# Optimization experiments

Hardware: AMD Instinct MI355X
Metric: run time of the kernel (lower is better)

Reference implementation:

```python
import jax, jax.numpy as jnp
import numpy as np

NUM_HEADS = 8
DIM = 256
SCALE = (DIM // NUM_HEADS) ** -0.5  # head_dim = dim // nhead = 32


def setup_inputs() -> dict:
    key = jax.random.key(0)
    k1, k2, k3, k4, k5 = jax.random.split(key, 5)
    B, N = 1, 4096
    qk = jax.random.normal(k1, (B, N, 3 * DIM), dtype=jnp.float32)
    v_cls = jax.random.normal(k2, (B, N, 2 * DIM), dtype=jnp.float32)
    masks = jax.random.uniform(k3, (B, N, N), dtype=jnp.float32)
    # torch Linear weights stored as [in, out] for x @ W
    W_qk = jax.random.normal(k4, (3 * DIM, 6 * DIM), dtype=jnp.float32) * (3 * DIM) ** -0.5
    W_v = jax.random.normal(k5, (2 * DIM, 2 * DIM), dtype=jnp.float32) * (2 * DIM) ** -0.5
    return {"qk": qk, "v_cls": v_cls, "masks": masks, "W_qk": W_qk, "W_v": W_v}


def reference(qk, v_cls, masks, W_qk, W_v):
    B, N, C_qk = qk.shape
    C_cls = v_cls.shape[-1]
    H = NUM_HEADS
    hd_qk = C_qk // H   # 96
    hd_v = C_cls // H   # 64

    # qk projection: [B,N,6*dim] -> (2,B,H,N,hd_qk)
    proj = (qk @ W_qk).reshape(B, N, 2, H, hd_qk).transpose(2, 0, 3, 1, 4)
    q, k = proj[0], proj[1]                      # [B,H,N,hd_qk]
    v = (v_cls @ W_v).reshape(B, N, H, hd_v).transpose(0, 2, 1, 3)  # [B,H,N,hd_v]

    attn = jnp.einsum('bhnd,bhmd->bhnm', q, k) * SCALE
    attn = jax.nn.softmax(attn, axis=-1)

    # post-softmax mask-mul and renorm by mask-sum and head count
    m = masks[:, None]                           # [B,1,N,N] broadcast over heads
    attn = attn * m / (H * jnp.sum(m, axis=-1, keepdims=True))
    # attn_drop with p=0.0 is identity in eval

    x_cls = jnp.einsum('bhnm,bhmd->bhnd', attn, v)
    return x_cls.transpose(0, 2, 1, 3).reshape(B, N, C_cls)
```

## Files before the change

### kernel.cpp

```cpp
#include <hip/hip_runtime.h>

typedef __attribute__((ext_vector_type(8))) _Float16 half8;
typedef __attribute__((ext_vector_type(4))) _Float16 half4;
typedef __attribute__((ext_vector_type(2))) _Float16 half2;
typedef __attribute__((ext_vector_type(2))) __fp16 fp16x2;
typedef __attribute__((ext_vector_type(4))) float f32x4;

#define N_SEQ 4096
#define HD_QK 96
#define HD_V  64
#define NHEADS 8
#define QSCALE 0.25505545556f
#define ESHIFT 8.0f

union PKC { fp16x2 p; half2 h; };

__device__ inline half2 pk_cvt(float a, float b) {
    PKC u;
    u.p = __builtin_amdgcn_cvt_pkrtz(a, b);
    return u.h;
}

__device__ inline half8 cvt8(float4 a, float4 b) {
    half8 h;
    h[0] = (_Float16)a.x; h[1] = (_Float16)a.y; h[2] = (_Float16)a.z; h[3] = (_Float16)a.w;
    h[4] = (_Float16)b.x; h[5] = (_Float16)b.y; h[6] = (_Float16)b.z; h[7] = (_Float16)b.w;
    return h;
}

__device__ inline void cast_blk(const float* __restrict__ in, _Float16* __restrict__ out,
                                int blk, int t) {
    size_t i = ((size_t)blk * 256 + t) * 8;
    float4 a = *(const float4*)(in + i);
    float4 b = *(const float4*)(in + i + 4);
    *(half8*)(out + i) = cvt8(a, b);
}

__global__ __launch_bounds__(256) void prep(
    const float* __restrict__ qk, const float* __restrict__ v_cls,
    const float* __restrict__ masks, const float* __restrict__ W_qk,
    const float* __restrict__ W_v,
    _Float16* __restrict__ Xh, _Float16* __restrict__ Vch,
    _Float16* __restrict__ Msw, float* __restrict__ Msum,
    _Float16* __restrict__ Wqkt, _Float16* __restrict__ Wvt)
{
    __shared__ float tile[32][33];
    const int bx = blockIdx.x, t = threadIdx.x;
    if (bx < 1536) {
        cast_blk(qk, Xh, bx, t);
    } else if (bx < 2560) {
        cast_blk(v_cls, Vch, bx - 1536, t);
    } else if (bx < 3968) {
        const bool big = bx < 3712;
        const int id = big ? bx - 2560 : bx - 3712;
        const int nx = big ? 48 : 16;
        const int C = big ? 1536 : 512, R = big ? 768 : 512;
        const float* in = big ? W_qk : W_v;
        _Float16* out = big ? Wqkt : Wvt;
        int cx = id % nx, cy = id / nx;
        int tx = t & 31, ty = t >> 5;
        int c0 = cx * 32, r0 = cy * 32;
        for (int k = 0; k < 4; k++)
            tile[ty + 8 * k][tx] = in[(size_t)(r0 + ty + 8 * k) * C + c0 + tx];
        __syncthreads();
        for (int k = 0; k < 4; k++)
            out[(size_t)(c0 + ty + 8 * k) * R + r0 + tx] = (_Float16)tile[tx][ty + 8 * k];
    } else {
        const int m = bx - 3968;
        const int q = m >> 1;
        const int k0 = (m & 1) * 2048 + t * 8;
        const float* src = masks + (size_t)q * N_SEQ + k0;
        float4 a = *(const float4*)src;
        float4 b = *(const float4*)(src + 4);
        const int q0b = q >> 6, l15 = q & 15, nt = (q >> 4) & 3;
        const int kb = k0 >> 6, wsl = (k0 >> 4) & 3, qd = (k0 >> 2) & 3;
        _Float16* dst = Msw + ((size_t)(q0b * 64 + kb) * 4 + wsl) * 1024
                            + l15 * 64 + qd * 16 + nt * 4;
        half4 h0 = {(_Float16)a.x, (_Float16)a.y, (_Float16)a.z, (_Float16)a.w};
        half4 h1 = {(_Float16)b.x, (_Float16)b.y, (_Float16)b.z, (_Float16)b.w};
        *(half4*)dst = h0;
        *(half4*)(dst + 16) = h1;
        float s = (a.x + a.y) + (a.z + a.w) + (b.x + b.y) + (b.z + b.w);
        for (int off = 1; off < 64; off <<= 1) s += __shfl_xor(s, off);
        if ((t & 63) == 0) atomicAdd(&Msum[q], s);
    }
}

__global__ __launch_bounds__(256) void proj_fused(
    const _Float16* __restrict__ Xh, const _Float16* __restrict__ Vch,
    const _Float16* __restrict__ Wqkt, const _Float16* __restrict__ Wvt,
    _Float16* __restrict__ Qh, _Float16* __restrict__ Kh,
    _Float16* __restrict__ Vtg)
{
    __shared__ _Float16 smem[2 * 128 * 72];
    _Float16 (*Xs)[72] = (_Float16 (*)[72])smem;
    _Float16 (*Ws)[72] = (_Float16 (*)[72])(smem + 128 * 72);

    const int t = threadIdx.x;
    const int lane = t & 63, wv = t >> 6;
    const int quad = lane >> 4, l15 = lane & 15;
    const bool qkmode = blockIdx.x < 12;
    const int n0 = qkmode ? blockIdx.x * 128 : (blockIdx.x - 12) * 128;
    const int row0 = blockIdx.y * 128;
    const int K = qkmode ? 768 : 512;
    const _Float16* X = qkmode ? Xh : Vch;
    const _Float16* Wt = qkmode ? Wqkt : Wvt;

    const int mB = (wv & 1) * 64, nB = (wv >> 1) * 64;
    const int sr = t >> 1, sk = (t & 1) * 32;

    const f32x4 fzero = {0.f, 0.f, 0.f, 0.f};
    f32x4 acc[4][4];
    for (int i = 0; i < 4; i++)
        for (int j = 0; j < 4; j++) acc[i][j] = fzero;

    for (int k0 = 0; k0 < K; k0 += 64) {
        __syncthreads();
        {
            const _Float16* xp = X + (size_t)(row0 + sr) * K + k0 + sk;
            *(half8*)&Xs[sr][sk]      = *(const half8*)xp;
            *(half8*)&Xs[sr][sk + 8]  = *(const half8*)(xp + 8);
            *(half8*)&Xs[sr][sk + 16] = *(const half8*)(xp + 16);
            *(half8*)&Xs[sr][sk + 24] = *(const half8*)(xp + 24);
            const _Float16* wp = Wt + (size_t)(n0 + sr) * K + k0 + sk;
            *(half8*)&Ws[sr][sk]      = *(const half8*)wp;
            *(half8*)&Ws[sr][sk + 8]  = *(const half8*)(wp + 8);
            *(half8*)&Ws[sr][sk + 16] = *(const half8*)(wp + 16);
            *(half8*)&Ws[sr][sk + 24] = *(const half8*)(wp + 24);
        }
        __syncthreads();
        for (int c = 0; c < 2; c++) {
            half8 af[4], bf[4];
            for (int i = 0; i < 4; i++)
                af[i] = *(const half8*)&Xs[mB + 16 * i + l15][c * 32 + quad * 8];
            for (int j = 0; j < 4; j++)
                bf[j] = *(const half8*)&Ws[nB + 16 * j + l15][c * 32 + quad * 8];
            for (int i = 0; i < 4; i++)
                for (int j = 0; j < 4; j++)
                    acc[i][j] = __builtin_amdgcn_mfma_f32_16x16x32_f16(af[i], bf[j], acc[i][j], 0, 0, 0);
        }
    }

    __syncthreads();
    _Float16 (*Ct)[136] = (_Float16 (*)[136])smem;
    for (int j = 0; j < 4; j++) {
        int col = n0 + nB + 16 * j + l15;
        float scl = (qkmode && col < 768) ? QSCALE : 1.0f;
        for (int i = 0; i < 4; i++)
            for (int r = 0; r < 4; r++)
                Ct[mB + 16 * i + quad * 4 + r][nB + 16 * j + l15] =
                    (_Float16)(acc[i][j][r] * scl);
    }
    __syncthreads();

    if (qkmode) {
        for (int e = 0; e < 8; e++) {
            int id = e * 256 + t;
            int row = id >> 4, cc = id & 15;
            int col = n0 + cc * 8;
            int w = col >= 768 ? 1 : 0;
            int rem = col - w * 768;
            int h = rem / 96, d = rem - h * 96;
            _Float16* dst = w ? Kh : Qh;
            *(half8*)&dst[((size_t)h * N_SEQ + row0 + row) * HD_QK + d] =
                *(const half8*)&Ct[row][cc * 8];
        }
    } else {
        for (int e = 0; e < 4; e++) {
            int id = e * 256 + t;
            int col = id >> 3, rc = id & 7;
            int c = n0 + col;
            int h = c >> 6, d = c & 63;
            half8 v0, v1;
            for (int k = 0; k < 8; k++) {
                v0[k] = Ct[rc * 16 + k][col];
                v1[k] = Ct[rc * 16 + 8 + k][col];
            }
            _Float16* dst = &Vtg[((size_t)h * HD_V + d) * N_SEQ + row0 + rc * 16];
            *(half8*)dst = v0;
            *(half8*)(dst + 8) = v1;
        }
    }
}

__global__ __launch_bounds__(256, 3) void flash_attn(
    const _Float16* __restrict__ Qh, const _Float16* __restrict__ Kh,
    const _Float16* __restrict__ Vtg, const _Float16* __restrict__ Msw,
    _Float16* __restrict__ Owsh, float* __restrict__ Lws)
{
    __shared__ __align__(16) float Ob[2][64][68];
    __shared__ float Lb[2][64];

    const int t = threadIdx.x;
    const int lane = t & 63, w = t >> 6;
    const int quad = lane >> 4, l15 = lane & 15;
    const int bx = blockIdx.x;
    const int q0b = bx & 63;
    const int hz = bx >> 6;
    const int head = hz & 7;
    const int z = hz >> 3;
    const int q0 = q0b * 64;
    const int kb0 = 21 * z, kbE = (z == 2) ? 64 : kb0 + 21;

    half8 qf[3][4];
    for (int nt = 0; nt < 4; nt++) {
        const _Float16* qp = Qh + ((size_t)head * N_SEQ + q0 + 16 * nt + l15) * HD_QK + 8 * quad;
        for (int c = 0; c < 3; c++)
            qf[c][nt] = *(const half8*)(qp + 32 * c);
    }

    const _Float16* kbase = Kh + ((size_t)head * N_SEQ + 16 * w + l15) * HD_QK + 8 * quad;
    const _Float16* vbase = Vtg + ((size_t)head * HD_V + l15) * N_SEQ + 16 * w + 4 * quad;
    const _Float16* mbase = Msw + ((size_t)(q0b * 64 + kb0) * 4 + w) * 1024
                                + (l15 * 4 + quad) * 16;

    const f32x4 fzero = {0.f, 0.f, 0.f, 0.f};
    f32x4 oacc[4][4];
    for (int nt = 0; nt < 4; nt++)
        for (int v = 0; v < 4; v++) oacc[nt][v] = fzero;
    float lsum[4] = {0.f, 0.f, 0.f, 0.f};

    half8 kf[3];
    half4 vf[4];
    half8 m01, m23;
    {
        const _Float16* kp = kbase + (size_t)kb0 * 64 * HD_QK;
        for (int c = 0; c < 3; c++) kf[c] = *(const half8*)(kp + 32 * c);
        const _Float16* vp = vbase + kb0 * 64;
        for (int v = 0; v < 4; v++) vf[v] = *(const half4*)(vp + (size_t)(16 * v) * N_SEQ);
        m01 = *(const half8*)mbase;
        m23 = *(const half8*)(mbase + 8);
    }

    for (int kb = kb0; kb < kbE; kb++) {
        const int kn = (kb + 1 < kbE) ? kb + 1 : kb;

        f32x4 sT[4];
        for (int nt = 0; nt < 4; nt++) sT[nt] = fzero;
        for (int c = 0; c < 3; c++)
            for (int nt = 0; nt < 4; nt++)
                sT[nt] = __builtin_amdgcn_mfma_f32_16x16x32_f16(kf[c], qf[c][nt], sT[nt], 0, 0, 0);
        {
            const _Float16* kp = kbase + (size_t)kn * 64 * HD_QK;
            for (int c = 0; c < 3; c++) kf[c] = *(const half8*)(kp + 32 * c);
        }

        half4 af[4];
        {
            half2 mh[8];
            for (int i = 0; i < 4; i++) {
                mh[i]     = half2{m01[2 * i], m01[2 * i + 1]};
                mh[4 + i] = half2{m23[2 * i], m23[2 * i + 1]};
            }
            for (int nt = 0; nt < 4; nt++) {
                float p0 = exp2f(sT[nt][0] - ESHIFT);
                float p1 = exp2f(sT[nt][1] - ESHIFT);
                float p2 = exp2f(sT[nt][2] - ESHIFT);
                float p3 = exp2f(sT[nt][3] - ESHIFT);
                lsum[nt] += (p0 + p1) + (p2 + p3);
                half2 lo = pk_cvt(p0, p1) * mh[2 * nt];
                half2 hi = pk_cvt(p2, p3) * mh[2 * nt + 1];
                af[nt] = half4{lo[0], lo[1], hi[0], hi[1]};
            }
        }
        {
            const _Float16* mp = mbase + (size_t)(kn - kb0) * 4096;
            m01 = *(const half8*)mp;
            m23 = *(const half8*)(mp + 8);
        }

        for (int nt = 0; nt < 4; nt++)
            for (int v = 0; v < 4; v++)
                oacc[nt][v] = __builtin_amdgcn_mfma_f32_16x16x16f16(af[nt], vf[v], oacc[nt][v], 0, 0, 0);
        {
            const _Float16* vp = vbase + kn * 64;
            for (int v = 0; v < 4; v++) vf[v] = *(const half4*)(vp + (size_t)(16 * v) * N_SEQ);
        }
    }

    for (int nt = 0; nt < 4; nt++) {
        lsum[nt] += __shfl_xor(lsum[nt], 16);
        lsum[nt] += __shfl_xor(lsum[nt], 32);
    }

    if (w & 1) {
        for (int nt = 0; nt < 4; nt++) {
            for (int v = 0; v < 4; v++)
                for (int r = 0; r < 4; r++)
                    Ob[w >> 1][16 * nt + 4 * quad + r][16 * v + l15] = oacc[nt][v][r];
            if (quad == 0) Lb[w >> 1][16 * nt + l15] = lsum[nt];
        }
    }
    __syncthreads();
    if (!(w & 1)) {
        for (int nt = 0; nt < 4; nt++) {
            for (int v = 0; v < 4; v++)
                for (int r = 0; r < 4; r++)
                    Ob[w >> 1][16 * nt + 4 * quad + r][16 * v + l15] += oacc[nt][v][r];
            if (quad == 0) Lb[w >> 1][16 * nt + l15] += lsum[nt];
        }
    }
    __syncthreads();

    {
        int row = t >> 2, c0 = (t & 3) * 16;
        _Float16* obase = Owsh + (size_t)z * N_SEQ * 512 + (size_t)(q0 + row) * 512
                          + head * HD_V + c0;
        for (int g = 0; g < 2; g++) {
            half8 h;
            for (int j = 0; j < 8; j++)
                h[j] = (_Float16)(Ob[0][row][c0 + 8 * g + j] + Ob[1][row][c0 + 8 * g + j]);
            *(half8*)(obase + 8 * g) = h;
        }
        if (t < 64)
            Lws[((size_t)z * NHEADS + head) * N_SEQ + q0 + t] = Lb[0][t] + Lb[1][t];
    }
}

__global__ __launch_bounds__(256) void finalize(
    const _Float16* __restrict__ Owsh, const float* __restrict__ Lws,
    const float* __restrict__ Msum, float* __restrict__ out)
{
    const size_t ZSTR = (size_t)N_SEQ * 512;
    size_t o = ((size_t)blockIdx.x * 256 + threadIdx.x) * 8;
    int q = (int)(o >> 9);
    int head = (int)((o & 511) >> 6);
    half8 p0 = *(const half8*)(Owsh + o);
    half8 p1 = *(const half8*)(Owsh + ZSTR + o);
    half8 p2 = *(const half8*)(Owsh + 2 * ZSTR + o);
    float l = Lws[(size_t)head * N_SEQ + q]
            + Lws[((size_t)NHEADS + head) * N_SEQ + q]
            + Lws[((size_t)2 * NHEADS + head) * N_SEQ + q];
    float inv = 1.0f / (l * (float)NHEADS * Msum[q]);
    float4 r0, r1;
    r0.x = ((float)p0[0] + (float)p1[0] + (float)p2[0]) * inv;
    r0.y = ((float)p0[1] + (float)p1[1] + (float)p2[1]) * inv;
    r0.z = ((float)p0[2] + (float)p1[2] + (float)p2[2]) * inv;
    r0.w = ((float)p0[3] + (float)p1[3] + (float)p2[3]) * inv;
    r1.x = ((float)p0[4] + (float)p1[4] + (float)p2[4]) * inv;
    r1.y = ((float)p0[5] + (float)p1[5] + (float)p2[5]) * inv;
    r1.z = ((float)p0[6] + (float)p1[6] + (float)p2[6]) * inv;
    r1.w = ((float)p0[7] + (float)p1[7] + (float)p2[7]) * inv;
    *(float4*)(out + o) = r0;
    *(float4*)(out + o + 4) = r1;
}

extern "C" void kernel_launch(void* const* d_in, const int* in_sizes, int n_in,
                              void* d_out, int out_size, void* d_ws, size_t ws_size,
                              hipStream_t stream) {
    const float* qk    = (const float*)d_in[0];
    const float* v_cls = (const float*)d_in[1];
    const float* masks = (const float*)d_in[2];
    const float* W_qk  = (const float*)d_in[3];
    const float* W_v   = (const float*)d_in[4];
    float* out = (float*)d_out;

    char* wsp = (char*)d_ws;
    _Float16* Xh   = (_Float16*)(wsp);
    _Float16* Vch  = (_Float16*)(wsp + (size_t)6291456);
    _Float16* Wqkt = (_Float16*)(wsp + (size_t)10485760);
    _Float16* Wvt  = (_Float16*)(wsp + (size_t)12845056);
    _Float16* Owsh = (_Float16*)(wsp);
    size_t off = 13631488;
    auto allocB = [&](size_t bytes) { char* p = wsp + off; off += (bytes + 255) & ~(size_t)255; return p; };
    _Float16* Qh   = (_Float16*)allocB((size_t)NHEADS * N_SEQ * HD_QK * 2);
    _Float16* Kh   = (_Float16*)allocB((size_t)NHEADS * N_SEQ * HD_QK * 2);
    _Float16* Vtg  = (_Float16*)allocB((size_t)NHEADS * HD_V * N_SEQ * 2);
    _Float16* Msw  = (_Float16*)allocB((size_t)N_SEQ * N_SEQ * 2);
    float*    Msum = (float*)allocB((size_t)N_SEQ * 4);
    float*    Lws  = (float*)allocB((size_t)3 * NHEADS * N_SEQ * 4);
    (void)ws_size;

    dim3 blk(256);
    (void)hipMemsetAsync(Msum, 0, N_SEQ * sizeof(float), stream);
    prep<<<dim3(12160), blk, 0, stream>>>(
        qk, v_cls, masks, W_qk, W_v, Xh, Vch, Msw, Msum, Wqkt, Wvt);

    proj_fused<<<dim3(16, N_SEQ / 128), blk, 0, stream>>>(
        Xh, Vch, Wqkt, Wvt, Qh, Kh, Vtg);

    flash_attn<<<dim3(1536), blk, 0, stream>>>(
        Qh, Kh, Vtg, Msw, Owsh, Lws);

    finalize<<<dim3((N_SEQ * 512) / (256 * 8)), blk, 0, stream>>>(
        Owsh, Lws, Msum, out);
}
```

Before: 281.5 us.

## Software-pipeline QK MFMA of next block with softmax and PV of previous block

Restructures the attention inner loop so the QK^T MFMAs for key block j run while exp/mask/PV work for block j-1 proceeds, using two ping-pong score register sets unrolled by two. This lets matrix-core work overlap the exp and convert ALU work. It also folds the exp shift into the MFMA accumulator init, dropping one subtract per element. The cost is an extra set of score registers, which adds pressure at the 3-waves launch bound.

```diff
diff --git a/kernel.cpp b/kernel.cpp
--- a/kernel.cpp
+++ b/kernel.cpp
@@ -183,6 +183,69 @@
     }
 }
 
+
+#define QK_MFMA(CUR)                                                          \
+    for (int c = 0; c < 3; c++)                                               \
+        for (int nt = 0; nt < 4; nt++)                                        \
+            CUR[nt] = __builtin_amdgcn_mfma_f32_16x16x32_f16(                 \
+                kf[c], qf[c][nt], (c == 0) ? minit : CUR[nt], 0, 0, 0);
+
+#define EXP_BLK(ST)                                                           \
+    {                                                                         \
+        half2 mh[8];                                                          \
+        for (int i = 0; i < 4; i++) {                                         \
+            mh[i]     = half2{m01[2 * i], m01[2 * i + 1]};                    \
+            mh[4 + i] = half2{m23[2 * i], m23[2 * i + 1]};                    \
+        }                                                                     \
+        for (int nt = 0; nt < 4; nt++) {                                      \
+            float p0 = exp2f(ST[nt][0]);                                      \
+            float p1 = exp2f(ST[nt][1]);                                      \
+            float p2 = exp2f(ST[nt][2]);                                      \
+            float p3 = exp2f(ST[nt][3]);                                      \
+            lsum[nt] += (p0 + p1) + (p2 + p3);                                \
+            half2 lo = pk_cvt(p0, p1) * mh[2 * nt];                           \
+            half2 hi = pk_cvt(p2, p3) * mh[2 * nt + 1];                       \
+            af[nt] = half4{lo[0], lo[1], hi[0], hi[1]};                       \
+        }                                                                     \
+    }
+
+#define PV_BLK                                                                \
+    for (int nt = 0; nt < 4; nt++)                                            \
+        for (int v = 0; v < 4; v++)                                           \
+            oacc[nt][v] = __builtin_amdgcn_mfma_f32_16x16x16f16(              \
+                af[nt], vf[v], oacc[nt][v], 0, 0, 0);
+
+#define STEP(CUR, PREV, J)                                                    \
+    do {                                                                      \
+        QK_MFMA(CUR);                                                         \
+        {                                                                     \
+            int kn_ = ((J) + 1 < kbE) ? (J) + 1 : (J);                        \
+            const _Float16* kp_ = kbase + (size_t)kn_ * 64 * HD_QK;           \
+            for (int c = 0; c < 3; c++)                                       \
+                kf[c] = *(const half8*)(kp_ + 32 * c);                        \
+        }                                                                     \
+        half4 af[4];                                                          \
+        EXP_BLK(PREV);                                                        \
+        {                                                                     \
+            const _Float16* mp_ = mbase + (size_t)((J) - kb0) * 4096;         \
+            m01 = *(const half8*)mp_;                                         \
+            m23 = *(const half8*)(mp_ + 8);                                   \
+        }                                                                     \
+        PV_BLK;                                                               \
+        {                                                                     \
+            const _Float16* vp_ = vbase + (J) * 64;                           \
+            for (int v = 0; v < 4; v++)                                       \
+                vf[v] = *(const half4*)(vp_ + (size_t)(16 * v) * N_SEQ);      \
+        }                                                                     \
+    } while (0)
+
+#define FINAL_BLK(ST)                                                         \
+    do {                                                                      \
+        half4 af[4];                                                          \
+        EXP_BLK(ST);                                                          \
+        PV_BLK;                                                               \
+    } while (0)
+
 __global__ __launch_bounds__(256, 3) void flash_attn(
     const _Float16* __restrict__ Qh, const _Float16* __restrict__ Kh,
     const _Float16* __restrict__ Vtg, const _Float16* __restrict__ Msw,
@@ -215,6 +278,7 @@
                                 + (l15 * 4 + quad) * 16;
 
     const f32x4 fzero = {0.f, 0.f, 0.f, 0.f};
+    const f32x4 minit = {-ESHIFT, -ESHIFT, -ESHIFT, -ESHIFT};
     f32x4 oacc[4][4];
     for (int nt = 0; nt < 4; nt++)
         for (int v = 0; v < 4; v++) oacc[nt][v] = fzero;
@@ -232,50 +296,24 @@
         m23 = *(const half8*)(mbase + 8);
     }
 
-    for (int kb = kb0; kb < kbE; kb++) {
-        const int kn = (kb + 1 < kbE) ? kb + 1 : kb;
-
-        f32x4 sT[4];
-        for (int nt = 0; nt < 4; nt++) sT[nt] = fzero;
-        for (int c = 0; c < 3; c++)
-            for (int nt = 0; nt < 4; nt++)
-                sT[nt] = __builtin_amdgcn_mfma_f32_16x16x32_f16(kf[c], qf[c][nt], sT[nt], 0, 0, 0);
-        {
-            const _Float16* kp = kbase + (size_t)kn * 64 * HD_QK;
-            for (int c = 0; c < 3; c++) kf[c] = *(const half8*)(kp + 32 * c);
-        }
-
-        half4 af[4];
-        {
-            half2 mh[8];
-            for (int i = 0; i < 4; i++) {
-                mh[i]     = half2{m01[2 * i], m01[2 * i + 1]};
-                mh[4 + i] = half2{m23[2 * i], m23[2 * i + 1]};
-            }
-            for (int nt = 0; nt < 4; nt++) {
-                float p0 = exp2f(sT[nt][0] - ESHIFT);
-                float p1 = exp2f(sT[nt][1] - ESHIFT);
-                float p2 = exp2f(sT[nt][2] - ESHIFT);
-                float p3 = exp2f(sT[nt][3] - ESHIFT);
-                lsum[nt] += (p0 + p1) + (p2 + p3);
-                half2 lo = pk_cvt(p0, p1) * mh[2 * nt];
-                half2 hi = pk_cvt(p2, p3) * mh[2 * nt + 1];
-                af[nt] = half4{lo[0], lo[1], hi[0], hi[1]};
-            }
-        }
-        {
-            const _Float16* mp = mbase + (size_t)(kn - kb0) * 4096;
-            m01 = *(const half8*)mp;
-            m23 = *(const half8*)(mp + 8);
-        }
-
-        for (int nt = 0; nt < 4; nt++)
-            for (int v = 0; v < 4; v++)
-                oacc[nt][v] = __builtin_amdgcn_mfma_f32_16x16x16f16(af[nt], vf[v], oacc[nt][v], 0, 0, 0);
-        {
-            const _Float16* vp = vbase + kn * 64;
-            for (int v = 0; v < 4; v++) vf[v] = *(const half4*)(vp + (size_t)(16 * v) * N_SEQ);
-        }
+    f32x4 sTA[4], sTB[4];
+    QK_MFMA(sTA);
+    {
+        const _Float16* kp = kbase + (size_t)(kb0 + 1) * 64 * HD_QK;
+        for (int c = 0; c < 3; c++) kf[c] = *(const half8*)(kp + 32 * c);
+    }
+
+    const int nsteps = kbE - kb0 - 1;
+    int j = kb0 + 1;
+    for (int s = 0; s + 1 < nsteps; s += 2) {
+        STEP(sTB, sTA, j); ++j;
+        STEP(sTA, sTB, j); ++j;
+    }
+    if (nsteps & 1) {
+        STEP(sTB, sTA, j);
+        FINAL_BLK(sTB);
+    } else {
+        FINAL_BLK(sTA);
     }
 
     for (int nt = 0; nt < 4; nt++) {
@@ -308,14 +346,20 @@
                           + head * HD_V + c0;
         for (int g = 0; g < 2; g++) {
             half8 h;
-            for (int j = 0; j < 8; j++)
-                h[j] = (_Float16)(Ob[0][row][c0 + 8 * g + j] + Ob[1][row][c0 + 8 * g + j]);
+            for (int j2 = 0; j2 < 8; j2++)
+                h[j2] = (_Float16)(Ob[0][row][c0 + 8 * g + j2] + Ob[1][row][c0 + 8 * g + j2]);
             *(half8*)(obase + 8 * g) = h;
         }
         if (t < 64)
             Lws[((size_t)z * NHEADS + head) * N_SEQ + q0 + t] = Lb[0][t] + Lb[1][t];
     }
 }
+
+#undef QK_MFMA
+#undef EXP_BLK
+#undef PV_BLK
+#undef STEP
+#undef FINAL_BLK
 
 __global__ __launch_bounds__(256) void finalize(
     const _Float16* __restrict__ Owsh, const float* __restrict__ Lws,
```

Result: slower. 454.2 us (+61.4%).

## Software-pipeline QK MFMA with softmax exp across key blocks, fold shift into init

Applied to the files above, without the earlier changes.

Restructures the attention loop so the QK^T MFMAs for the next key block are issued while the exp/mask work of the current block runs, using a prologue and epilogue. The exp shift is folded into the MFMA accumulator initial value, which removes a subtraction per element. Explicit unroll pragmas are added throughout. This is meant to hide MFMA latency behind VALU transcendental work, at the cost of extra live registers for a second score tile.

```diff
diff --git a/kernel.cpp b/kernel.cpp
--- a/kernel.cpp
+++ b/kernel.cpp
@@ -203,8 +203,10 @@
     const int kb0 = 21 * z, kbE = (z == 2) ? 64 : kb0 + 21;
 
     half8 qf[3][4];
+#pragma unroll
     for (int nt = 0; nt < 4; nt++) {
         const _Float16* qp = Qh + ((size_t)head * N_SEQ + q0 + 16 * nt + l15) * HD_QK + 8 * quad;
+#pragma unroll
         for (int c = 0; c < 3; c++)
             qf[c][nt] = *(const half8*)(qp + 32 * c);
     }
@@ -215,8 +217,11 @@
                                 + (l15 * 4 + quad) * 16;
 
     const f32x4 fzero = {0.f, 0.f, 0.f, 0.f};
+    const f32x4 minit = {-ESHIFT, -ESHIFT, -ESHIFT, -ESHIFT};
     f32x4 oacc[4][4];
+#pragma unroll
     for (int nt = 0; nt < 4; nt++)
+#pragma unroll
         for (int v = 0; v < 4; v++) oacc[nt][v] = fzero;
     float lsum[4] = {0.f, 0.f, 0.f, 0.f};
 
@@ -225,57 +230,100 @@
     half8 m01, m23;
     {
         const _Float16* kp = kbase + (size_t)kb0 * 64 * HD_QK;
+#pragma unroll
         for (int c = 0; c < 3; c++) kf[c] = *(const half8*)(kp + 32 * c);
         const _Float16* vp = vbase + kb0 * 64;
+#pragma unroll
         for (int v = 0; v < 4; v++) vf[v] = *(const half4*)(vp + (size_t)(16 * v) * N_SEQ);
         m01 = *(const half8*)mbase;
         m23 = *(const half8*)(mbase + 8);
     }
 
-    for (int kb = kb0; kb < kbE; kb++) {
-        const int kn = (kb + 1 < kbE) ? kb + 1 : kb;
-
-        f32x4 sT[4];
-        for (int nt = 0; nt < 4; nt++) sT[nt] = fzero;
-        for (int c = 0; c < 3; c++)
-            for (int nt = 0; nt < 4; nt++)
-                sT[nt] = __builtin_amdgcn_mfma_f32_16x16x32_f16(kf[c], qf[c][nt], sT[nt], 0, 0, 0);
+    f32x4 sT[4];
+#pragma unroll
+    for (int nt = 0; nt < 4; nt++) {
+        f32x4 s = __builtin_amdgcn_mfma_f32_16x16x32_f16(kf[0], qf[0][nt], minit, 0, 0, 0);
+        s = __builtin_amdgcn_mfma_f32_16x16x32_f16(kf[1], qf[1][nt], s, 0, 0, 0);
+        s = __builtin_amdgcn_mfma_f32_16x16x32_f16(kf[2], qf[2][nt], s, 0, 0, 0);
+        sT[nt] = s;
+    }
+    {
+        const _Float16* kp = kbase + (size_t)(kb0 + 1) * 64 * HD_QK;
+#pragma unroll
+        for (int c = 0; c < 3; c++) kf[c] = *(const half8*)(kp + 32 * c);
+    }
+
+    for (int j = kb0 + 1; j < kbE; j++) {
+        half4 af[4];
+        half2 mh[8];
+#pragma unroll
+        for (int i = 0; i < 4; i++) {
+            mh[i]     = half2{m01[2 * i], m01[2 * i + 1]};
+            mh[4 + i] = half2{m23[2 * i], m23[2 * i + 1]};
+        }
+#pragma unroll
+        for (int nt = 0; nt < 4; nt++) {
+            f32x4 s = __builtin_amdgcn_mfma_f32_16x16x32_f16(kf[0], qf[0][nt], minit, 0, 0, 0);
+            s = __builtin_amdgcn_mfma_f32_16x16x32_f16(kf[1], qf[1][nt], s, 0, 0, 0);
+            s = __builtin_amdgcn_mfma_f32_16x16x32_f16(kf[2], qf[2][nt], s, 0, 0, 0);
+            float p0 = exp2f(sT[nt][0]);
+            float p1 = exp2f(sT[nt][1]);
+            float p2 = exp2f(sT[nt][2]);
+            float p3 = exp2f(sT[nt][3]);
+            lsum[nt] += (p0 + p1) + (p2 + p3);
+            half2 lo = pk_cvt(p0, p1) * mh[2 * nt];
+            half2 hi = pk_cvt(p2, p3) * mh[2 * nt + 1];
+            af[nt] = half4{lo[0], lo[1], hi[0], hi[1]};
+            sT[nt] = s;
+        }
         {
+            int kn = (j + 1 < kbE) ? j + 1 : j;
             const _Float16* kp = kbase + (size_t)kn * 64 * HD_QK;
+#pragma unroll
             for (int c = 0; c < 3; c++) kf[c] = *(const half8*)(kp + 32 * c);
         }
-
-        half4 af[4];
         {
-            half2 mh[8];
-            for (int i = 0; i < 4; i++) {
-                mh[i]     = half2{m01[2 * i], m01[2 * i + 1]};
-                mh[4 + i] = half2{m23[2 * i], m23[2 * i + 1]};
-            }
-            for (int nt = 0; nt < 4; nt++) {
-                float p0 = exp2f(sT[nt][0] - ESHIFT);
-                float p1 = exp2f(sT[nt][1] - ESHIFT);
-                float p2 = exp2f(sT[nt][2] - ESHIFT);
-                float p3 = exp2f(sT[nt][3] - ESHIFT);
-                lsum[nt] += (p0 + p1) + (p2 + p3);
-                half2 lo = pk_cvt(p0, p1) * mh[2 * nt];
-                half2 hi = pk_cvt(p2, p3) * mh[2 * nt + 1];
-                af[nt] = half4{lo[0], lo[1], hi[0], hi[1]};
-            }
-        }
-        {
-            const _Float16* mp = mbase + (size_t)(kn - kb0) * 4096;
+            const _Float16* mp = mbase + (size_t)(j - kb0) * 4096;
             m01 = *(const half8*)mp;
             m23 = *(const half8*)(mp + 8);
         }
-
+#pragma unroll
         for (int nt = 0; nt < 4; nt++)
+#pragma unroll
             for (int v = 0; v < 4; v++)
                 oacc[nt][v] = __builtin_amdgcn_mfma_f32_16x16x16f16(af[nt], vf[v], oacc[nt][v], 0, 0, 0);
         {
-            const _Float16* vp = vbase + kn * 64;
-            for (int v = 0; v < 4; v++) vf[v] = *(const half4*)(vp + (size_t)(16 * v) * N_SEQ);
-        }
+            const _Float16* vp = vbase + (size_t)j * 64;
+#pragma unroll
+            for (int v = 0; v < 4; v++)
+                vf[v] = *(const half4*)(vp + (size_t)(16 * v) * N_SEQ);
+        }
+    }
+
+    {
+        half4 af[4];
+        half2 mh[8];
+#pragma unroll
+        for (int i = 0; i < 4; i++) {
+            mh[i]     = half2{m01[2 * i], m01[2 * i + 1]};
+            mh[4 + i] = half2{m23[2 * i], m23[2 * i + 1]};
+        }
+#pragma unroll
+        for (int nt = 0; nt < 4; nt++) {
+            float p0 = exp2f(sT[nt][0]);
+            float p1 = exp2f(sT[nt][1]);
+            float p2 = exp2f(sT[nt][2]);
+            float p3 = exp2f(sT[nt][3]);
+            lsum[nt] += (p0 + p1) + (p2 + p3);
+            half2 lo = pk_cvt(p0, p1) * mh[2 * nt];
+            half2 hi = pk_cvt(p2, p3) * mh[2 * nt + 1];
+            af[nt] = half4{lo[0], lo[1], hi[0], hi[1]};
+        }
+#pragma unroll
+        for (int nt = 0; nt < 4; nt++)
+#pragma unroll
+            for (int v = 0; v < 4; v++)
+                oacc[nt][v] = __builtin_amdgcn_mfma_f32_16x16x16f16(af[nt], vf[v], oacc[nt][v], 0, 0, 0);
     }
 
     for (int nt = 0; nt < 4; nt++) {
@@ -308,8 +356,8 @@
                           + head * HD_V + c0;
         for (int g = 0; g < 2; g++) {
             half8 h;
-            for (int j = 0; j < 8; j++)
-                h[j] = (_Float16)(Ob[0][row][c0 + 8 * g + j] + Ob[1][row][c0 + 8 * g + j]);
+            for (int j2 = 0; j2 < 8; j2++)
+                h[j2] = (_Float16)(Ob[0][row][c0 + 8 * g + j2] + Ob[1][row][c0 + 8 * g + j2]);
             *(half8*)(obase + 8 * g) = h;
         }
         if (t < 64)
```

After: 310.8 us. 10.4% more time.

## Double-buffer K/V/mask register prefetch two blocks ahead and fold shift into MFMA init

Applied to the files above, without the earlier changes.

Restructures the attention inner loop to keep two register sets of K, V and mask fragments, loading block j+2 while computing block j, with the loop unrolled by two and a remainder step. The -ESHIFT subtraction is folded into the QK accumulator's initial value, and the three QK MFMAs per tile are chained per nt. The aim is to hide global-load latency behind more compute. The extra registers may reduce occupancy at the launch bound of 3 blocks per CU or cause spills.

```diff
diff --git a/kernel.cpp b/kernel.cpp
--- a/kernel.cpp
+++ b/kernel.cpp
@@ -183,6 +183,60 @@
     }
 }
 
+
+#define FA_ITER(KF, VF, M01, M23, J)                                          \
+    do {                                                                      \
+        f32x4 sT[4];                                                          \
+        for (int nt = 0; nt < 4; nt++) {                                      \
+            f32x4 s = __builtin_amdgcn_mfma_f32_16x16x32_f16(KF[0], qf[0][nt], minit, 0, 0, 0); \
+            s = __builtin_amdgcn_mfma_f32_16x16x32_f16(KF[1], qf[1][nt], s, 0, 0, 0); \
+            s = __builtin_amdgcn_mfma_f32_16x16x32_f16(KF[2], qf[2][nt], s, 0, 0, 0); \
+            sT[nt] = s;                                                       \
+        }                                                                     \
+        {                                                                     \
+            const int kn_ = ((J) + 2 < kbE) ? (J) + 2 : kbE - 1;              \
+            const _Float16* kp_ = kbase + (size_t)kn_ * 64 * HD_QK;           \
+            KF[0] = *(const half8*)kp_;                                       \
+            KF[1] = *(const half8*)(kp_ + 32);                                \
+            KF[2] = *(const half8*)(kp_ + 64);                                \
+        }                                                                     \
+        half4 af[4];                                                          \
+        {                                                                     \
+            half2 mh[8];                                                      \
+            for (int i = 0; i < 4; i++) {                                     \
+                mh[i]     = half2{M01[2 * i], M01[2 * i + 1]};                \
+                mh[4 + i] = half2{M23[2 * i], M23[2 * i + 1]};                \
+            }                                                                 \
+            for (int nt = 0; nt < 4; nt++) {                                  \
+                float p0 = exp2f(sT[nt][0]);                                  \
+                float p1 = exp2f(sT[nt][1]);                                  \
+                float p2 = exp2f(sT[nt][2]);                                  \
+                float p3 = exp2f(sT[nt][3]);                                  \
+                lsum[nt] += (p0 + p1) + (p2 + p3);                            \
+                half2 lo = pk_cvt(p0, p1) * mh[2 * nt];                       \
+                half2 hi = pk_cvt(p2, p3) * mh[2 * nt + 1];                   \
+                af[nt] = half4{lo[0], lo[1], hi[0], hi[1]};                   \
+            }                                                                 \
+        }                                                                     \
+        {                                                                     \
+            const int kn_ = ((J) + 2 < kbE) ? (J) + 2 : kbE - 1;              \
+            const _Float16* mp_ = mbase + (size_t)(kn_ - kb0) * 4096;         \
+            M01 = *(const half8*)mp_;                                         \
+            M23 = *(const half8*)(mp_ + 8);                                   \
+        }                                                                     \
+        for (int nt = 0; nt < 4; nt++)                                        \
+            for (int v = 0; v < 4; v++)                                       \
+                oacc[nt][v] = __builtin_amdgcn_mfma_f32_16x16x16f16(af[nt], VF[v], oacc[nt][v], 0, 0, 0); \
+        {                                                                     \
+            const int kn_ = ((J) + 2 < kbE) ? (J) + 2 : kbE - 1;              \
+            const _Float16* vp_ = vbase + (size_t)kn_ * 64;                   \
+            VF[0] = *(const half4*)vp_;                                       \
+            VF[1] = *(const half4*)(vp_ + (size_t)16 * N_SEQ);                \
+            VF[2] = *(const half4*)(vp_ + (size_t)32 * N_SEQ);                \
+            VF[3] = *(const half4*)(vp_ + (size_t)48 * N_SEQ);                \
+        }                                                                     \
+    } while (0)
+
 __global__ __launch_bounds__(256, 3) void flash_attn(
     const _Float16* __restrict__ Qh, const _Float16* __restrict__ Kh,
     const _Float16* __restrict__ Vtg, const _Float16* __restrict__ Msw,
@@ -215,67 +269,50 @@
                                 + (l15 * 4 + quad) * 16;
 
     const f32x4 fzero = {0.f, 0.f, 0.f, 0.f};
+    const f32x4 minit = {-ESHIFT, -ESHIFT, -ESHIFT, -ESHIFT};
     f32x4 oacc[4][4];
     for (int nt = 0; nt < 4; nt++)
         for (int v = 0; v < 4; v++) oacc[nt][v] = fzero;
     float lsum[4] = {0.f, 0.f, 0.f, 0.f};
 
-    half8 kf[3];
-    half4 vf[4];
-    half8 m01, m23;
+    half8 kfA[3], kfB[3];
+    half4 vfA[4], vfB[4];
+    half8 mA01, mA23, mB01, mB23;
     {
         const _Float16* kp = kbase + (size_t)kb0 * 64 * HD_QK;
-        for (int c = 0; c < 3; c++) kf[c] = *(const half8*)(kp + 32 * c);
-        const _Float16* vp = vbase + kb0 * 64;
-        for (int v = 0; v < 4; v++) vf[v] = *(const half4*)(vp + (size_t)(16 * v) * N_SEQ);
-        m01 = *(const half8*)mbase;
-        m23 = *(const half8*)(mbase + 8);
-    }
-
-    for (int kb = kb0; kb < kbE; kb++) {
-        const int kn = (kb + 1 < kbE) ? kb + 1 : kb;
-
-        f32x4 sT[4];
-        for (int nt = 0; nt < 4; nt++) sT[nt] = fzero;
-        for (int c = 0; c < 3; c++)
-            for (int nt = 0; nt < 4; nt++)
-                sT[nt] = __builtin_amdgcn_mfma_f32_16x16x32_f16(kf[c], qf[c][nt], sT[nt], 0, 0, 0);
-        {
-            const _Float16* kp = kbase + (size_t)kn * 64 * HD_QK;
-            for (int c = 0; c < 3; c++) kf[c] = *(const half8*)(kp + 32 * c);
-        }
-
-        half4 af[4];
-        {
-            half2 mh[8];
-            for (int i = 0; i < 4; i++) {
-                mh[i]     = half2{m01[2 * i], m01[2 * i + 1]};
-                mh[4 + i] = half2{m23[2 * i], m23[2 * i + 1]};
-            }
-            for (int nt = 0; nt < 4; nt++) {
-                float p0 = exp2f(sT[nt][0] - ESHIFT);
-                float p1 = exp2f(sT[nt][1] - ESHIFT);
-                float p2 = exp2f(sT[nt][2] - ESHIFT);
-                float p3 = exp2f(sT[nt][3] - ESHIFT);
-                lsum[nt] += (p0 + p1) + (p2 + p3);
-                half2 lo = pk_cvt(p0, p1) * mh[2 * nt];
-                half2 hi = pk_cvt(p2, p3) * mh[2 * nt + 1];
-                af[nt] = half4{lo[0], lo[1], hi[0], hi[1]};
-            }
-        }
-        {
-            const _Float16* mp = mbase + (size_t)(kn - kb0) * 4096;
-            m01 = *(const half8*)mp;
-            m23 = *(const half8*)(mp + 8);
-        }
-
-        for (int nt = 0; nt < 4; nt++)
-            for (int v = 0; v < 4; v++)
-                oacc[nt][v] = __builtin_amdgcn_mfma_f32_16x16x16f16(af[nt], vf[v], oacc[nt][v], 0, 0, 0);
-        {
-            const _Float16* vp = vbase + kn * 64;
-            for (int v = 0; v < 4; v++) vf[v] = *(const half4*)(vp + (size_t)(16 * v) * N_SEQ);
-        }
+        kfA[0] = *(const half8*)kp;
+        kfA[1] = *(const half8*)(kp + 32);
+        kfA[2] = *(const half8*)(kp + 64);
+        const _Float16* vp = vbase + (size_t)kb0 * 64;
+        vfA[0] = *(const half4*)vp;
+        vfA[1] = *(const half4*)(vp + (size_t)16 * N_SEQ);
+        vfA[2] = *(const half4*)(vp + (size_t)32 * N_SEQ);
+        vfA[3] = *(const half4*)(vp + (size_t)48 * N_SEQ);
+        mA01 = *(const half8*)mbase;
+        mA23 = *(const half8*)(mbase + 8);
+    }
+    {
+        const _Float16* kp = kbase + (size_t)(kb0 + 1) * 64 * HD_QK;
+        kfB[0] = *(const half8*)kp;
+        kfB[1] = *(const half8*)(kp + 32);
+        kfB[2] = *(const half8*)(kp + 64);
+        const _Float16* vp = vbase + (size_t)(kb0 + 1) * 64;
+        vfB[0] = *(const half4*)vp;
+        vfB[1] = *(const half4*)(vp + (size_t)16 * N_SEQ);
+        vfB[2] = *(const half4*)(vp + (size_t)32 * N_SEQ);
+        vfB[3] = *(const half4*)(vp + (size_t)48 * N_SEQ);
+        const _Float16* mp = mbase + 4096;
+        mB01 = *(const half8*)mp;
+        mB23 = *(const half8*)(mp + 8);
+    }
+
+    int j = kb0;
+    for (; j + 1 < kbE; j += 2) {
+        FA_ITER(kfA, vfA, mA01, mA23, j);
+        FA_ITER(kfB, vfB, mB01, mB23, j + 1);
+    }
+    if (j < kbE) {
+        FA_ITER(kfA, vfA, mA01, mA23, j);
     }
 
     for (int nt = 0; nt < 4; nt++) {
@@ -308,14 +345,16 @@
                           + head * HD_V + c0;
         for (int g = 0; g < 2; g++) {
             half8 h;
-            for (int j = 0; j < 8; j++)
-                h[j] = (_Float16)(Ob[0][row][c0 + 8 * g + j] + Ob[1][row][c0 + 8 * g + j]);
+            for (int j2 = 0; j2 < 8; j2++)
+                h[j2] = (_Float16)(Ob[0][row][c0 + 8 * g + j2] + Ob[1][row][c0 + 8 * g + j2]);
             *(half8*)(obase + 8 * g) = h;
         }
         if (t < 64)
             Lws[((size_t)z * NHEADS + head) * N_SEQ + q0 + t] = Lb[0][t] + Lb[1][t];
     }
 }
+
+#undef FA_ITER
 
 __global__ __launch_bounds__(256) void finalize(
     const _Float16* __restrict__ Owsh, const float* __restrict__ Lws,
```

Result: slower. 437.6 us (+55.4%).
